# Kernel tuning notes

Measured on AMD Instinct MI355X. Metric: run time of the kernel, lower is better.

Reference implementation:

```python
import jax, jax.numpy as jnp
import numpy as np

B = 64          # batch of vectors to apply the HODLR operator to
N = 262144      # num_nodes = 2**18, divisible by 2**depth
DEPTH = 8       # hierarchy depth -> 2**(i+1) blocks at level i
RANK = 64       # low-rank off-diagonal rank


def setup_inputs() -> dict:
    key = jax.random.key(0)
    kx, ku = jax.random.split(key)
    x = jax.random.normal(kx, (B, N, 1), dtype=jnp.float32)
    # learned parameters per DirectHODLR.__init__
    diag = jnp.ones((1, N, 1), dtype=jnp.float32)              # self.diag
    u = jax.random.normal(ku, (DEPTH, N, RANK), dtype=jnp.float32) * 0.001  # stacked u_factors
    return {"x": x, "diag": diag, "u": u}


def reference(x, diag, u):
    """HODLR matvec: y = diag*x + sum over levels of symmetric off-diagonal
    low-rank sibling exchange. At level i the node axis is split into 2**(i+1)
    blocks; each adjacent pair (left, right) contributes
        y_left  += U_left  @ (U_right^T x_right)
        y_right += U_right @ (U_left^T  x_left)
    """
    Bn, Nn, _ = x.shape
    y = diag * x
    depth = u.shape[0]
    for i in range(depth):
        nb = 2 ** (i + 1)           # number of blocks at this level
        bs = Nn // nb               # block size
        # [pairs, 2(sibling), block, rank]
        ub = u[i].reshape(nb // 2, 2, bs, -1)
        # [batch, pairs, 2, block]
        xb = x.reshape(Bn, nb // 2, 2, bs)
        # project each sibling block onto its low-rank basis: [b, p, s, r]
        t = jnp.einsum('pscr,bpsc->bpsr', ub, xb)
        # exchange siblings (off-diagonal coupling)
        ts = t[:, :, ::-1]
        # expand back to node space and accumulate
        y = y + jnp.einsum('pscr,bpsr->bpsc', ub, ts).reshape(Bn, Nn, 1)
    return y
```

## Files before the change

kernel.cpp:

```cpp
#include <hip/hip_runtime.h>


typedef __attribute__((ext_vector_type(8))) short bf16x8;
typedef __attribute__((ext_vector_type(4))) float f32x4;

constexpr int BATCH = 64;
constexpr int NN    = 262144;
constexpr int RANK  = 64;
constexpr int DEPTH = 8;
constexpr int CHUNK = 256;
constexpr int NCHUNK = NN / CHUNK;
constexpr int NWG  = NCHUNK;
constexpr int NTHR = 256;
constexpr int LSTR  = 264;
constexpr int WIN   = 256;
constexpr size_t TS_FLOATS = 510ull * 4096;
constexpr int BARSTRIDE = 256;

__device__ __forceinline__ short f2bf(float f) {
  union { float f; unsigned u; } v; v.f = f;
  unsigned r = v.u + 0x7FFFu + ((v.u >> 16) & 1u);
  return (short)(r >> 16);
}

__device__ __forceinline__ float bf2f(short s) {
  union { unsigned u; float f; } v; v.u = ((unsigned)(unsigned short)s) << 16;
  return v.f;
}

__device__ __forceinline__ bf16x8 pack8(f32x4 a, f32x4 b) {
  bf16x8 f;
  f[0] = f2bf(a[0]); f[1] = f2bf(a[1]); f[2] = f2bf(a[2]); f[3] = f2bf(a[3]);
  f[4] = f2bf(b[0]); f[5] = f2bf(b[1]); f[6] = f2bf(b[2]); f[7] = f2bf(b[3]);
  return f;
}

__device__ __forceinline__ unsigned short aload_u16(const unsigned short* p) {
  return __hip_atomic_load(p, __ATOMIC_RELAXED, __HIP_MEMORY_SCOPE_AGENT);
}
__device__ __forceinline__ float aload_f32(const float* p) {
  return __hip_atomic_load(p, __ATOMIC_RELAXED, __HIP_MEMORY_SCOPE_AGENT);
}
__device__ __forceinline__ void astore_u16(unsigned short* p, unsigned short v) {
  __hip_atomic_store(p, v, __ATOMIC_RELAXED, __HIP_MEMORY_SCOPE_AGENT);
}
__device__ __forceinline__ void astore_f32(float* p, float v) {
  __hip_atomic_store(p, v, __ATOMIC_RELAXED, __HIP_MEMORY_SCOPE_AGENT);
}

__device__ __forceinline__ int rowoff(int r) { return r * 264 + ((r >> 3) << 3); }

__device__ __forceinline__ void gbar3(unsigned* bars, unsigned ph) {
  __syncthreads();
  const int tid = threadIdx.x;
  if (blockIdx.x == 0) {
    if (tid == 0)
      __hip_atomic_fetch_add(bars, 1u, __ATOMIC_RELAXED, __HIP_MEMORY_SCOPE_AGENT);
    if (tid < 64) {
      unsigned* a = bars + tid * BARSTRIDE;
      while (__hip_atomic_load(a, __ATOMIC_RELAXED, __HIP_MEMORY_SCOPE_AGENT) < ph * 16u)
        __builtin_amdgcn_s_sleep(1);
    }
    __syncthreads();
    if (tid < 64)
      __hip_atomic_store(bars + (64 + tid) * BARSTRIDE, ph,
                         __ATOMIC_RELAXED, __HIP_MEMORY_SCOPE_AGENT);
    __syncthreads();
  } else {
    if (tid == 0) {
      __hip_atomic_fetch_add(bars + (blockIdx.x & 63) * BARSTRIDE, 1u,
                             __ATOMIC_RELAXED, __HIP_MEMORY_SCOPE_AGENT);
      unsigned* r = bars + (64 + (blockIdx.x & 63)) * BARSTRIDE;
      while (__hip_atomic_load(r, __ATOMIC_RELAXED, __HIP_MEMORY_SCOPE_AGENT) < ph)
        __builtin_amdgcn_s_sleep(4);
    }
    __syncthreads();
  }
}

__global__ __launch_bounds__(256, 4) void k_fused3(
    const float* __restrict__ x, const float* __restrict__ diag,
    const float* __restrict__ u, float* y,
    short* part, float* ts, unsigned* bars, float* s1)
{
  __shared__ alignas(16) short ulds[64 * 264 + 64];

  const int c0   = blockIdx.x * CHUNK;
  const int tid  = threadIdx.x;
  const int w    = tid >> 6;
  const int lane = tid & 63;
  const int lg   = lane >> 4;
  const int lr   = lane & 15;
  const int bw   = 16 * w;
  const int T    = blockIdx.x * NTHR + tid;

  bf16x8 xf[CHUNK / 32];
  {
    const float* xp = x + (size_t)(bw + lr) * NN + c0 + lg * 8;
    #pragma unroll
    for (int s = 0; s < CHUNK / 32; ++s) {
      f32x4 a = *(const f32x4*)(xp + s * 32);
      f32x4 b = *(const f32x4*)(xp + s * 32 + 4);
      xf[s] = pack8(a, b);
    }
  }

  f32x4 yacc[16];
  #pragma unroll
  for (int ct = 0; ct < 16; ++ct) yacc[ct] = (f32x4){0.f, 0.f, 0.f, 0.f};

  unsigned ph = 0;

  #pragma unroll 1
  for (int i = 0; i < DEPTH; ++i) {
    __syncthreads();

    {
      const float* ug = u + ((size_t)i * NN + c0 + tid) * RANK;
      #pragma unroll
      for (int h = 0; h < 4; ++h) {
        f32x4 t[4];
        #pragma unroll
        for (int q = 0; q < 4; ++q) t[q] = *(const f32x4*)(ug + h * 16 + q * 4);
        #pragma unroll
        for (int q = 0; q < 4; ++q) {
          #pragma unroll
          for (int e = 0; e < 4; ++e) {
            const int r = h * 16 + q * 4 + e;
            ulds[rowoff(r) + tid] = f2bf(t[q][e]);
          }
        }
      }
    }
    __syncthreads();

    {
      unsigned short* pb = (unsigned short*)(part +
          ((size_t)i * NCHUNK + blockIdx.x) * (BATCH * RANK));
      #pragma unroll
      for (int rt = 0; rt < 4; ++rt) {
        f32x4 pacc = (f32x4){0.f, 0.f, 0.f, 0.f};
        const int rbase = rowoff(rt * 16 + lr);
        #pragma unroll
        for (int s = 0; s < CHUNK / 32; ++s) {
          bf16x8 bf = *(const bf16x8*)&ulds[rbase + s * 32 + lg * 8];
          pacc = __builtin_amdgcn_mfma_f32_16x16x32_bf16(xf[s], bf, pacc, 0, 0, 0);
        }
        #pragma unroll
        for (int v = 0; v < 4; ++v)
          astore_u16(pb + (bw + lg * 4 + v) * RANK + rt * 16 + lr,
                     (unsigned short)f2bf(pacc[v]));
      }
    }

    gbar3(bars, ++ph);

    {
      const int contrib = 512 >> i;
      const int tsbase  = ((1 << (i + 1)) - 2) * (BATCH * RANK);
      const unsigned short* pl = (const unsigned short*)(part +
          (size_t)i * NCHUNK * (BATCH * RANK));
      if (i <= 2) {
        const int entries = 1 << (13 + i);
        const int G       = 32 >> i;
        const int e   = T & (entries - 1);
        const int grp = T >> (13 + i);
        const int blk = e >> 12, br = e & 4095;
        const unsigned short* p = pl + (size_t)(blk * contrib + grp * 16) * 4096 + br;
        float s = 0.f;
        #pragma unroll
        for (int k = 0; k < 16; ++k) s += bf2f((short)aload_u16(p + (size_t)k * 4096));
        astore_f32(&s1[(size_t)grp * entries + e], s);

        gbar3(bars, ++ph);

        if (T < entries) {
          float s2 = 0.f;
          #pragma unroll 8
          for (int g2 = 0; g2 < G; ++g2)
            s2 += aload_f32(&s1[(size_t)g2 * entries + T]);
          astore_f32(&ts[tsbase + T], s2);
        }
      } else if (i <= 4) {
        const int entries = 1 << (13 + i);
        if (T < entries) {
          const int blk = T >> 12, br = T & 4095;
          const unsigned short* p = pl + (size_t)(blk * contrib) * 4096 + br;
          float s = 0.f;
          for (int k0 = 0; k0 < contrib; k0 += 16) {
            #pragma unroll
            for (int k = 0; k < 16; ++k)
              s += bf2f((short)aload_u16(p + (size_t)(k0 + k) * 4096));
          }
          astore_f32(&ts[tsbase + T], s);
        }
      } else {
        const int units = 1 << (i - 5);
        for (int uu = 0; uu < units; ++uu) {
          const int e = T + (uu << 18);
          const int blk = e >> 12, br = e & 4095;
          const unsigned short* p = pl + (size_t)(blk * contrib) * 4096 + br;
          float s = 0.f;
          #pragma unroll
          for (int k = 0; k < 16; ++k)
            if (k < contrib) s += bf2f((short)aload_u16(p + (size_t)k * 4096));
          astore_f32(&ts[tsbase + e], s);
        }
      }
    }

    gbar3(bars, ++ph);

    {
      const int blk = c0 >> (17 - i);
      const float* tb = ts + (size_t)(((1 << (i + 1)) - 2) + (blk ^ 1)) * (BATCH * RANK);

      bf16x8 af[2];
      #pragma unroll
      for (int s2 = 0; s2 < 2; ++s2) {
        const float* p = tb + (size_t)(bw + lr) * RANK + s2 * 32 + lg * 8;
        f32x4 a, b;
        #pragma unroll
        for (int j = 0; j < 4; ++j) {
          a[j] = aload_f32(p + j);
          b[j] = aload_f32(p + 4 + j);
        }
        af[s2] = pack8(a, b);
      }

      #pragma unroll
      for (int ct = 0; ct < 16; ++ct) {
        #pragma unroll
        for (int s2 = 0; s2 < 2; ++s2) {
          const int rb = rowoff(s2 * 32 + lg * 8);
          bf16x8 bf;
          #pragma unroll
          for (int j = 0; j < 8; ++j)
            bf[j] = ulds[rb + j * 264 + ct * 16 + lr];
          yacc[ct] = __builtin_amdgcn_mfma_f32_16x16x32_bf16(af[s2], bf, yacc[ct], 0, 0, 0);
        }
      }
    }
  }

  #pragma unroll
  for (int ct = 0; ct < 16; ++ct) {
    const int c = c0 + ct * 16 + lr;
    const float dg = diag[c];
    #pragma unroll
    for (int v = 0; v < 4; ++v) {
      const int b = bw + lg * 4 + v;
      const size_t idx = (size_t)b * NN + c;
      y[idx] = yacc[ct][v] + dg * x[idx];
    }
  }
}


__global__ __launch_bounds__(256, 4) void k_proj2(
    const float* __restrict__ x, const float* __restrict__ u,
    short* __restrict__ part)
{
  __shared__ alignas(16) short ulds[RANK * LSTR];

  const int c0   = blockIdx.x * CHUNK;
  const int tid  = threadIdx.x;
  const int w    = tid >> 6;
  const int lane = tid & 63;
  const int lg   = lane >> 4;
  const int lr   = lane & 15;

  bf16x8 xf[CHUNK / 32];
  {
    const float* xp = x + (size_t)(16 * w + lr) * NN + c0 + lg * 8;
    #pragma unroll
    for (int s = 0; s < CHUNK / 32; ++s) {
      f32x4 a = *(const f32x4*)(xp + s * 32);
      f32x4 b = *(const f32x4*)(xp + s * 32 + 4);
      xf[s] = pack8(a, b);
    }
  }

  for (int i = 0; i < DEPTH; ++i) {
    __syncthreads();
    {
      const float* ug = u + ((size_t)i * NN + c0 + tid) * RANK;
      short* col = &ulds[tid];
      #pragma unroll
      for (int h = 0; h < 2; ++h) {
        f32x4 t[8];
        #pragma unroll
        for (int q = 0; q < 8; ++q) t[q] = *(const f32x4*)(ug + h * 32 + q * 4);
        #pragma unroll
        for (int q = 0; q < 8; ++q) {
          #pragma unroll
          for (int e = 0; e < 4; ++e)
            col[(h * 32 + q * 4 + e) * LSTR] = f2bf(t[q][e]);
        }
      }
    }
    __syncthreads();

    f32x4 pacc[4];
    #pragma unroll
    for (int rt = 0; rt < 4; ++rt) pacc[rt] = (f32x4){0.f, 0.f, 0.f, 0.f};
    #pragma unroll
    for (int s = 0; s < CHUNK / 32; ++s) {
      #pragma unroll
      for (int rt = 0; rt < 4; ++rt) {
        bf16x8 bf = *(const bf16x8*)&ulds[(rt * 16 + lr) * LSTR + s * 32 + lg * 8];
        pacc[rt] = __builtin_amdgcn_mfma_f32_16x16x32_bf16(xf[s], bf, pacc[rt], 0, 0, 0);
      }
    }

    short* pb = part + ((size_t)i * NCHUNK + blockIdx.x) * (BATCH * RANK);
    #pragma unroll
    for (int rt = 0; rt < 4; ++rt) {
      #pragma unroll
      for (int v = 0; v < 4; ++v) {
        const int b = 16 * w + lg * 4 + v;
        pb[b * RANK + rt * 16 + lr] = f2bf(pacc[rt][v]);
      }
    }
  }
}

__global__ __launch_bounds__(256, 4) void k_reduce(
    const short* __restrict__ part, float* __restrict__ ts)
{
  int g = blockIdx.x;
  int lvl = 0;
  while (g >= ((2 << lvl) * 16)) { g -= (2 << lvl) * 16; ++lvl; }
  const int block = g >> 4;
  const int bq = (g >> 2) & 3;
  const int rq = g & 3;
  const int contrib = 512 >> lvl;
  const int chunk0  = block * contrib;

  const int b = bq * 16 + (threadIdx.x >> 4);
  const int r = rq * 16 + (threadIdx.x & 15);

  const short* p = part + ((size_t)lvl * NCHUNK + chunk0) * (BATCH * RANK) + b * RANK + r;
  float s = 0.f;
  int k = 0;
  for (; k + 8 <= contrib; k += 8) {
    float a0 = bf2f(p[(size_t)(k + 0) * 4096]);
    float a1 = bf2f(p[(size_t)(k + 1) * 4096]);
    float a2 = bf2f(p[(size_t)(k + 2) * 4096]);
    float a3 = bf2f(p[(size_t)(k + 3) * 4096]);
    float a4 = bf2f(p[(size_t)(k + 4) * 4096]);
    float a5 = bf2f(p[(size_t)(k + 5) * 4096]);
    float a6 = bf2f(p[(size_t)(k + 6) * 4096]);
    float a7 = bf2f(p[(size_t)(k + 7) * 4096]);
    s += ((a0 + a1) + (a2 + a3)) + ((a4 + a5) + (a6 + a7));
  }
  for (; k < contrib; ++k) s += bf2f(p[(size_t)k * 4096]);

  const int off = (1 << (lvl + 1)) - 2;
  ts[(size_t)(off + block) * (BATCH * RANK) + b * RANK + r] = s;
}

__global__ __launch_bounds__(256, 4) void k_exp2(
    const float* __restrict__ x, const float* __restrict__ diag,
    const float* __restrict__ u, const float* __restrict__ ts,
    float* __restrict__ y)
{
  const int cw0  = blockIdx.x * WIN;
  const int tid  = threadIdx.x;
  const int w    = tid >> 6;
  const int lane = tid & 63;
  const int lg   = lane >> 4;
  const int lr   = lane & 15;
  const int bw   = 16 * w;

  f32x4 yacc[16];
  #pragma unroll
  for (int ct = 0; ct < 16; ++ct) yacc[ct] = (f32x4){0.f, 0.f, 0.f, 0.f};

  #pragma unroll
  for (int i = 0; i < DEPTH; ++i) {
    const int blk = cw0 >> (17 - i);
    const int off = (1 << (i + 1)) - 2;
    const float* tb = ts + (size_t)(off + (blk ^ 1)) * (BATCH * RANK);

    bf16x8 af[2];
    #pragma unroll
    for (int s2 = 0; s2 < 2; ++s2) {
      const float* p = tb + (size_t)(bw + lr) * RANK + s2 * 32 + lg * 8;
      af[s2] = pack8(*(const f32x4*)p, *(const f32x4*)(p + 4));
    }

    const float* ub = u + ((size_t)i * NN + cw0) * RANK;
    #pragma unroll
    for (int ct = 0; ct < 16; ++ct) {
      const float* up = ub + (size_t)(ct * 16 + lr) * RANK + lg * 8;
      #pragma unroll
      for (int s2 = 0; s2 < 2; ++s2) {
        f32x4 a = *(const f32x4*)(up + s2 * 32);
        f32x4 b = *(const f32x4*)(up + s2 * 32 + 4);
        yacc[ct] = __builtin_amdgcn_mfma_f32_16x16x32_bf16(af[s2], pack8(a, b), yacc[ct], 0, 0, 0);
      }
    }
  }

  #pragma unroll
  for (int ct = 0; ct < 16; ++ct) {
    const int c = cw0 + ct * 16 + lr;
    const float dg = diag[c];
    #pragma unroll
    for (int v = 0; v < 4; ++v) {
      const int b = bw + lg * 4 + v;
      const size_t idx = (size_t)b * NN + c;
      y[idx] = yacc[ct][v] + dg * x[idx];
    }
  }
}

extern "C" void kernel_launch(void* const* d_in, const int* in_sizes, int n_in,
                              void* d_out, int out_size, void* d_ws, size_t ws_size,
                              hipStream_t stream) {
  (void)in_sizes; (void)n_in; (void)out_size; (void)ws_size;
  const float* x    = (const float*)d_in[0];
  const float* diag = (const float*)d_in[1];
  const float* u    = (const float*)d_in[2];
  float* y    = (float*)d_out;
  short* part = (short*)d_out;
  float* ts   = (float*)d_ws;

  char* wsb = (char*)d_ws;
  unsigned* bars = (unsigned*)(wsb + TS_FLOATS * 4);
  float*    s1   = (float*)(wsb + TS_FLOATS * 4 + 128 * BARSTRIDE * 4);

  hipMemsetAsync(wsb + TS_FLOATS * 4, 0, 128 * BARSTRIDE * 4, stream);

  void* args[8] = {(void*)&x, (void*)&diag, (void*)&u, (void*)&y,
                   (void*)&part, (void*)&ts, (void*)&bars, (void*)&s1};
  if (hipLaunchCooperativeKernel((const void*)k_fused3, dim3(NWG), dim3(NTHR),
                                 args, 0, stream) != hipSuccess) {
    k_proj2 <<<NCHUNK, 256, 0, stream>>>(x, u, part);
    k_reduce<<<8160,   256, 0, stream>>>(part, ts);
    k_exp2  <<<NN / WIN, 256, 0, stream>>>(x, diag, u, ts, y);
  }
}
```

Baseline: 488.6 us.

## Software-pipeline levels with per-event flags instead of global barriers

Replaces the hierarchical grid barrier with per-level event counters (release/acquire), then skews the level loop so projection of level j, reduction of level j-1 and expansion of level j-2 run in one iteration. Blocks only wait on the specific event each stage depends on. This lets projection work overlap with reduction and expansion instead of serialising every level behind full barriers. Because LDS now holds a different level's U during expansion, expansion re-reads U from global memory and converts it to bf16 again. The scratch s1 buffer now lives in unused ts space.

```diff
diff --git a/kernel.cpp b/kernel.cpp
--- a/kernel.cpp
+++ b/kernel.cpp
@@ -15,7 +15,12 @@
 constexpr int LSTR  = 264;
 constexpr int WIN   = 256;
 constexpr size_t TS_FLOATS = 510ull * 4096;
-constexpr int BARSTRIDE = 256;
+
+constexpr int EV_P  = 0;
+constexpr int EV_R1 = 8;
+constexpr int EV_R2 = 11;
+constexpr int NEV   = 19;
+constexpr int FLINE = 32;
 
 __device__ __forceinline__ short f2bf(float f) {
   union { float f; unsigned u; } v; v.f = f;
@@ -50,38 +55,29 @@
 
 __device__ __forceinline__ int rowoff(int r) { return r * 264 + ((r >> 3) << 3); }
 
-__device__ __forceinline__ void gbar3(unsigned* bars, unsigned ph) {
+__device__ __forceinline__ void arrive_ev(unsigned* flags, int ev) {
   __syncthreads();
-  const int tid = threadIdx.x;
-  if (blockIdx.x == 0) {
-    if (tid == 0)
-      __hip_atomic_fetch_add(bars, 1u, __ATOMIC_RELAXED, __HIP_MEMORY_SCOPE_AGENT);
-    if (tid < 64) {
-      unsigned* a = bars + tid * BARSTRIDE;
-      while (__hip_atomic_load(a, __ATOMIC_RELAXED, __HIP_MEMORY_SCOPE_AGENT) < ph * 16u)
-        __builtin_amdgcn_s_sleep(1);
-    }
-    __syncthreads();
-    if (tid < 64)
-      __hip_atomic_store(bars + (64 + tid) * BARSTRIDE, ph,
-                         __ATOMIC_RELAXED, __HIP_MEMORY_SCOPE_AGENT);
-    __syncthreads();
-  } else {
-    if (tid == 0) {
-      __hip_atomic_fetch_add(bars + (blockIdx.x & 63) * BARSTRIDE, 1u,
-                             __ATOMIC_RELAXED, __HIP_MEMORY_SCOPE_AGENT);
-      unsigned* r = bars + (64 + (blockIdx.x & 63)) * BARSTRIDE;
-      while (__hip_atomic_load(r, __ATOMIC_RELAXED, __HIP_MEMORY_SCOPE_AGENT) < ph)
-        __builtin_amdgcn_s_sleep(4);
-    }
-    __syncthreads();
-  }
-}
-
-__global__ __launch_bounds__(256, 4) void k_fused3(
+  if (threadIdx.x == 0)
+    __hip_atomic_fetch_add(flags + (ev * 64 + (blockIdx.x & 63)) * FLINE, 1u,
+                           __ATOMIC_RELEASE, __HIP_MEMORY_SCOPE_AGENT);
+}
+__device__ __forceinline__ void wait_ev(unsigned* flags, int ev) {
+  if (threadIdx.x < 64) {
+    const unsigned* a = flags + (ev * 64 + threadIdx.x) * FLINE;
+    int it = 0;
+    while (__hip_atomic_load(a, __ATOMIC_ACQUIRE, __HIP_MEMORY_SCOPE_AGENT) < 16u) {
+      if (it < 16) __builtin_amdgcn_s_sleep(2);
+      else         __builtin_amdgcn_s_sleep(8);
+      ++it;
+    }
+  }
+  __syncthreads();
+}
+
+__global__ __launch_bounds__(256, 4) void k_fused4(
     const float* __restrict__ x, const float* __restrict__ diag,
     const float* __restrict__ u, float* y,
-    short* part, float* ts, unsigned* bars, float* s1)
+    short* part, float* ts, unsigned* flags)
 {
   __shared__ alignas(16) short ulds[64 * 264 + 64];
 
@@ -109,71 +105,110 @@
   #pragma unroll
   for (int ct = 0; ct < 16; ++ct) yacc[ct] = (f32x4){0.f, 0.f, 0.f, 0.f};
 
-  unsigned ph = 0;
-
   #pragma unroll 1
-  for (int i = 0; i < DEPTH; ++i) {
-    __syncthreads();
+  for (int j = 0; j < DEPTH + 2; ++j) {
+
+    if (j < DEPTH) {
+      __syncthreads();
+      {
+        const float* ug = u + ((size_t)j * NN + c0 + tid) * RANK;
+        #pragma unroll
+        for (int h = 0; h < 4; ++h) {
+          f32x4 t[4];
+          #pragma unroll
+          for (int q = 0; q < 4; ++q) t[q] = *(const f32x4*)(ug + h * 16 + q * 4);
+          #pragma unroll
+          for (int q = 0; q < 4; ++q) {
+            #pragma unroll
+            for (int e = 0; e < 4; ++e) {
+              const int r = h * 16 + q * 4 + e;
+              ulds[rowoff(r) + tid] = f2bf(t[q][e]);
+            }
+          }
+        }
+      }
+      __syncthreads();
+
+      {
+        unsigned short* pb = (unsigned short*)(part +
+            ((size_t)j * NCHUNK + blockIdx.x) * (BATCH * RANK));
+        #pragma unroll
+        for (int rt = 0; rt < 4; ++rt) {
+          f32x4 pacc = (f32x4){0.f, 0.f, 0.f, 0.f};
+          const int rbase = rowoff(rt * 16 + lr);
+          #pragma unroll
+          for (int s = 0; s < CHUNK / 32; ++s) {
+            bf16x8 bf = *(const bf16x8*)&ulds[rbase + s * 32 + lg * 8];
+            pacc = __builtin_amdgcn_mfma_f32_16x16x32_bf16(xf[s], bf, pacc, 0, 0, 0);
+          }
+          #pragma unroll
+          for (int v = 0; v < 4; ++v)
+            astore_u16(pb + (bw + lg * 4 + v) * RANK + rt * 16 + lr,
+                       (unsigned short)f2bf(pacc[v]));
+        }
+      }
+      arrive_ev(flags, EV_P + j);
+    }
 
     {
-      const float* ug = u + ((size_t)i * NN + c0 + tid) * RANK;
-      #pragma unroll
-      for (int h = 0; h < 4; ++h) {
-        f32x4 t[4];
-        #pragma unroll
-        for (int q = 0; q < 4; ++q) t[q] = *(const f32x4*)(ug + h * 16 + q * 4);
-        #pragma unroll
-        for (int q = 0; q < 4; ++q) {
-          #pragma unroll
-          for (int e = 0; e < 4; ++e) {
-            const int r = h * 16 + q * 4 + e;
-            ulds[rowoff(r) + tid] = f2bf(t[q][e]);
-          }
-        }
-      }
-    }
-    __syncthreads();
+      const int L = j - 1;
+      if (L >= 0 && L < DEPTH) {
+        wait_ev(flags, EV_P + L);
+        const int contrib = 512 >> L;
+        const int tsbase  = ((1 << (L + 1)) - 2) * (BATCH * RANK);
+        const unsigned short* pl = (const unsigned short*)(part +
+            (size_t)L * NCHUNK * (BATCH * RANK));
+        if (L <= 2) {
+          float* s1 = ts + ((size_t)(1 << (8 - L)) - 2) * (BATCH * RANK);
+          const int entries = 1 << (13 + L);
+          const int e   = T & (entries - 1);
+          const int grp = T >> (13 + L);
+          const int blk = e >> 12, br = e & 4095;
+          const unsigned short* p = pl + (size_t)(blk * contrib + grp * 16) * 4096 + br;
+          float s = 0.f;
+          #pragma unroll
+          for (int k = 0; k < 16; ++k) s += bf2f((short)aload_u16(p + (size_t)k * 4096));
+          astore_f32(&s1[(size_t)grp * entries + e], s);
+          arrive_ev(flags, EV_R1 + L);
+        } else if (L <= 4) {
+          const int entries = 1 << (13 + L);
+          if (T < entries) {
+            const int blk = T >> 12, br = T & 4095;
+            const unsigned short* p = pl + (size_t)(blk * contrib) * 4096 + br;
+            float s = 0.f;
+            for (int k0 = 0; k0 < contrib; k0 += 16) {
+              #pragma unroll
+              for (int k = 0; k < 16; ++k)
+                s += bf2f((short)aload_u16(p + (size_t)(k0 + k) * 4096));
+            }
+            astore_f32(&ts[tsbase + T], s);
+          }
+          arrive_ev(flags, EV_R2 + L);
+        } else {
+          const int units = 1 << (L - 5);
+          for (int uu = 0; uu < units; ++uu) {
+            const int e = T + (uu << 18);
+            const int blk = e >> 12, br = e & 4095;
+            const unsigned short* p = pl + (size_t)(blk * contrib) * 4096 + br;
+            float s = 0.f;
+            #pragma unroll
+            for (int k = 0; k < 16; ++k)
+              if (k < contrib) s += bf2f((short)aload_u16(p + (size_t)k * 4096));
+            astore_f32(&ts[tsbase + e], s);
+          }
+          arrive_ev(flags, EV_R2 + L);
+        }
+      }
+    }
 
     {
-      unsigned short* pb = (unsigned short*)(part +
-          ((size_t)i * NCHUNK + blockIdx.x) * (BATCH * RANK));
-      #pragma unroll
-      for (int rt = 0; rt < 4; ++rt) {
-        f32x4 pacc = (f32x4){0.f, 0.f, 0.f, 0.f};
-        const int rbase = rowoff(rt * 16 + lr);
-        #pragma unroll
-        for (int s = 0; s < CHUNK / 32; ++s) {
-          bf16x8 bf = *(const bf16x8*)&ulds[rbase + s * 32 + lg * 8];
-          pacc = __builtin_amdgcn_mfma_f32_16x16x32_bf16(xf[s], bf, pacc, 0, 0, 0);
-        }
-        #pragma unroll
-        for (int v = 0; v < 4; ++v)
-          astore_u16(pb + (bw + lg * 4 + v) * RANK + rt * 16 + lr,
-                     (unsigned short)f2bf(pacc[v]));
-      }
-    }
-
-    gbar3(bars, ++ph);
-
-    {
-      const int contrib = 512 >> i;
-      const int tsbase  = ((1 << (i + 1)) - 2) * (BATCH * RANK);
-      const unsigned short* pl = (const unsigned short*)(part +
-          (size_t)i * NCHUNK * (BATCH * RANK));
-      if (i <= 2) {
-        const int entries = 1 << (13 + i);
-        const int G       = 32 >> i;
-        const int e   = T & (entries - 1);
-        const int grp = T >> (13 + i);
-        const int blk = e >> 12, br = e & 4095;
-        const unsigned short* p = pl + (size_t)(blk * contrib + grp * 16) * 4096 + br;
-        float s = 0.f;
-        #pragma unroll
-        for (int k = 0; k < 16; ++k) s += bf2f((short)aload_u16(p + (size_t)k * 4096));
-        astore_f32(&s1[(size_t)grp * entries + e], s);
-
-        gbar3(bars, ++ph);
-
+      const int L2 = j - 2;
+      if (L2 >= 0 && L2 <= 2) {
+        wait_ev(flags, EV_R1 + L2);
+        const float* s1 = ts + ((size_t)(1 << (8 - L2)) - 2) * (BATCH * RANK);
+        const int tsbase  = ((1 << (L2 + 1)) - 2) * (BATCH * RANK);
+        const int entries = 1 << (13 + L2);
+        const int G       = 32 >> L2;
         if (T < entries) {
           float s2 = 0.f;
           #pragma unroll 8
@@ -181,63 +216,41 @@
             s2 += aload_f32(&s1[(size_t)g2 * entries + T]);
           astore_f32(&ts[tsbase + T], s2);
         }
-      } else if (i <= 4) {
-        const int entries = 1 << (13 + i);
-        if (T < entries) {
-          const int blk = T >> 12, br = T & 4095;
-          const unsigned short* p = pl + (size_t)(blk * contrib) * 4096 + br;
-          float s = 0.f;
-          for (int k0 = 0; k0 < contrib; k0 += 16) {
-            #pragma unroll
-            for (int k = 0; k < 16; ++k)
-              s += bf2f((short)aload_u16(p + (size_t)(k0 + k) * 4096));
-          }
-          astore_f32(&ts[tsbase + T], s);
-        }
-      } else {
-        const int units = 1 << (i - 5);
-        for (int uu = 0; uu < units; ++uu) {
-          const int e = T + (uu << 18);
-          const int blk = e >> 12, br = e & 4095;
-          const unsigned short* p = pl + (size_t)(blk * contrib) * 4096 + br;
-          float s = 0.f;
-          #pragma unroll
-          for (int k = 0; k < 16; ++k)
-            if (k < contrib) s += bf2f((short)aload_u16(p + (size_t)k * 4096));
-          astore_f32(&ts[tsbase + e], s);
-        }
-      }
-    }
-
-    gbar3(bars, ++ph);
+        arrive_ev(flags, EV_R2 + L2);
+      }
+    }
 
     {
-      const int blk = c0 >> (17 - i);
-      const float* tb = ts + (size_t)(((1 << (i + 1)) - 2) + (blk ^ 1)) * (BATCH * RANK);
-
-      bf16x8 af[2];
-      #pragma unroll
-      for (int s2 = 0; s2 < 2; ++s2) {
-        const float* p = tb + (size_t)(bw + lr) * RANK + s2 * 32 + lg * 8;
-        f32x4 a, b;
-        #pragma unroll
-        for (int j = 0; j < 4; ++j) {
-          a[j] = aload_f32(p + j);
-          b[j] = aload_f32(p + 4 + j);
-        }
-        af[s2] = pack8(a, b);
-      }
-
-      #pragma unroll
-      for (int ct = 0; ct < 16; ++ct) {
+      const int L2 = j - 2;
+      if (L2 >= 0 && L2 < DEPTH) {
+        wait_ev(flags, EV_R2 + L2);
+        const int blk = c0 >> (17 - L2);
+        const float* tb = ts + (size_t)(((1 << (L2 + 1)) - 2) + (blk ^ 1)) * (BATCH * RANK);
+
+        bf16x8 af[2];
         #pragma unroll
         for (int s2 = 0; s2 < 2; ++s2) {
-          const int rb = rowoff(s2 * 32 + lg * 8);
-          bf16x8 bf;
-          #pragma unroll
-          for (int j = 0; j < 8; ++j)
-            bf[j] = ulds[rb + j * 264 + ct * 16 + lr];
-          yacc[ct] = __builtin_amdgcn_mfma_f32_16x16x32_bf16(af[s2], bf, yacc[ct], 0, 0, 0);
+          const float* p = tb + (size_t)(bw + lr) * RANK + s2 * 32 + lg * 8;
+          f32x4 a, b;
+          #pragma unroll
+          for (int jj = 0; jj < 4; ++jj) {
+            a[jj] = aload_f32(p + jj);
+            b[jj] = aload_f32(p + 4 + jj);
+          }
+          af[s2] = pack8(a, b);
+        }
+
+        const float* ub = u + ((size_t)L2 * NN + c0) * RANK;
+        #pragma unroll
+        for (int ct = 0; ct < 16; ++ct) {
+          const float* up = ub + (size_t)(ct * 16 + lr) * RANK + lg * 8;
+          #pragma unroll
+          for (int s2 = 0; s2 < 2; ++s2) {
+            f32x4 a = *(const f32x4*)(up + s2 * 32);
+            f32x4 b = *(const f32x4*)(up + s2 * 32 + 4);
+            yacc[ct] = __builtin_amdgcn_mfma_f32_16x16x32_bf16(af[s2], pack8(a, b),
+                                                               yacc[ct], 0, 0, 0);
+          }
         }
       }
     }
@@ -428,14 +441,13 @@
   float* ts   = (float*)d_ws;
 
   char* wsb = (char*)d_ws;
-  unsigned* bars = (unsigned*)(wsb + TS_FLOATS * 4);
-  float*    s1   = (float*)(wsb + TS_FLOATS * 4 + 128 * BARSTRIDE * 4);
-
-  hipMemsetAsync(wsb + TS_FLOATS * 4, 0, 128 * BARSTRIDE * 4, stream);
-
-  void* args[8] = {(void*)&x, (void*)&diag, (void*)&u, (void*)&y,
-                   (void*)&part, (void*)&ts, (void*)&bars, (void*)&s1};
-  if (hipLaunchCooperativeKernel((const void*)k_fused3, dim3(NWG), dim3(NTHR),
+  unsigned* flags = (unsigned*)(wsb + TS_FLOATS * 4);
+
+  (void)hipMemsetAsync(wsb + TS_FLOATS * 4, 0, (size_t)NEV * 64 * FLINE * 4, stream);
+
+  void* args[7] = {(void*)&x, (void*)&diag, (void*)&u, (void*)&y,
+                   (void*)&part, (void*)&ts, (void*)&flags};
+  if (hipLaunchCooperativeKernel((const void*)k_fused4, dim3(NWG), dim3(NTHR),
                                  args, 0, stream) != hipSuccess) {
     k_proj2 <<<NCHUNK, 256, 0, stream>>>(x, u, part);
     k_reduce<<<8160,   256, 0, stream>>>(part, ts);
```

Result: slower. 1.785 ms (+265.4%).
